# Performance work log

Measured on AMD Instinct MI355X. Metric: run time of the kernel, lower is better.

## Reference

```python
import jax, jax.numpy as jnp
import numpy as np


def setup_inputs() -> dict:
    key = jax.random.key(0)
    k1, k2, k3 = jax.random.split(key, 3)
    B, T, S, D = 8, 2048, 2048, 512
    main_input = jax.random.normal(k1, (B, T, D), dtype=jnp.float32)
    attn_input = jax.random.normal(k2, (B, S, D), dtype=jnp.float32)
    # f_input is a torch Linear(D, D): y = x @ W_f.T + b_f
    W_f = jax.random.normal(k3, (D, D), dtype=jnp.float32) * (1.0 / np.sqrt(D))
    b_f = jnp.zeros((D,), dtype=jnp.float32)
    return {"main_input": main_input, "attn_input": attn_input, "W_f": W_f, "b_f": b_f}


def reference(main_input, attn_input, W_f, b_f):
    # keys: f_input applied to each attn word  [B,S,D]
    keys = jnp.einsum("bsd,ed->bse", attn_input, W_f) + b_f
    # scores[b,t,s] = keys[b,s,:] . main_input[b,t,:]
    scores = jnp.einsum("bse,bte->bts", keys, main_input)
    attn = jax.nn.softmax(scores, axis=-1)  # softmax over attn words S
    # weighted sum of RAW attn_input (values are unprojected)
    out = jnp.einsum("bts,bsd->btd", attn, attn_input)
    return out
```

## Files before the change

### kernel.cpp

```cpp
#include <hip/hip_runtime.h>
#include <math.h>

#define B_  8
#define T_  2048
#define S_  2048
#define D_  512

typedef _Float16 half8   __attribute__((ext_vector_type(8)));
typedef _Float16 half4_t __attribute__((ext_vector_type(4)));
typedef float    floatx4 __attribute__((ext_vector_type(4)));

__device__ __forceinline__ floatx4 mfma16(half8 a, half8 b, floatx4 c) {
  return __builtin_amdgcn_mfma_f32_16x16x32_f16(a, b, c, 0, 0, 0);
}

__device__ __forceinline__ void async16(void* lds, const void* g) {
  __builtin_amdgcn_global_load_lds(
      (const __attribute__((address_space(1))) void*)g,
      (__attribute__((address_space(3))) void*)lds, 16, 0, 0);
}

__device__ __forceinline__ void bar_lds() {
  __builtin_amdgcn_sched_barrier(0);
  asm volatile("s_waitcnt lgkmcnt(0)" ::: "memory");
  __builtin_amdgcn_s_barrier();
  __builtin_amdgcn_sched_barrier(0);
}

__global__ __launch_bounds__(256) void transpose_cast_kernel(
    const float* __restrict__ attn, _Float16* __restrict__ Vt) {
  __shared__ _Float16 tile[32][33];
  const int tx = threadIdx.x, ty = threadIdx.y;
  const int b = blockIdx.z, s0 = blockIdx.y * 32, d0 = blockIdx.x * 32;
  const float* src = attn + ((size_t)b * S_ + s0) * D_ + d0;
#pragma unroll
  for (int i = 0; i < 4; ++i) {
    int s = ty + i * 8;
    tile[tx][s] = (_Float16)src[(size_t)s * D_ + tx];
  }
  __syncthreads();
  _Float16* dst = Vt + ((size_t)b * D_ + d0) * S_ + s0;
#pragma unroll
  for (int i = 0; i < 4; ++i) {
    int d = ty + i * 8;
    dst[(size_t)d * S_ + tx] = tile[d][tx];
  }
}

__global__ __launch_bounds__(512, 2) void keys_gemm_kernel(
    const float* __restrict__ X, const float* __restrict__ W,
    const float* __restrict__ bias, _Float16* __restrict__ K16) {
  __shared__ alignas(16) _Float16 Xs[128][72];
  __shared__ alignas(16) _Float16 Ws[128][72];
  const int t = threadIdx.x;
  const int wave = t >> 6, lane = t & 63, q = lane >> 4, n = lane & 15;
  const int wm = wave >> 2, wn = wave & 3;
  const int m0 = blockIdx.x * 128, n0 = blockIdx.y * 128;

  floatx4 acc[4][2];
#pragma unroll
  for (int i = 0; i < 4; ++i)
#pragma unroll
    for (int j = 0; j < 2; ++j) {
      floatx4 z = {0.f, 0.f, 0.f, 0.f};
      acc[i][j] = z;
    }

  for (int kc = 0; kc < 8; ++kc) {
    const int k0 = kc * 64;
#pragma unroll
    for (int i = 0; i < 4; ++i) {
      int seg = i * 512 + t;
      int row = seg >> 4, c4 = (seg & 15) * 4;
      floatx4 xv = *(const floatx4*)&X[(size_t)(m0 + row) * D_ + k0 + c4];
      floatx4 wv = *(const floatx4*)&W[(size_t)(n0 + row) * D_ + k0 + c4];
      half4_t xh, wh;
#pragma unroll
      for (int j = 0; j < 4; ++j) { xh[j] = (_Float16)xv[j]; wh[j] = (_Float16)wv[j]; }
      *(half4_t*)&Xs[row][c4] = xh;
      *(half4_t*)&Ws[row][c4] = wh;
    }
    __syncthreads();
#pragma unroll
    for (int kk = 0; kk < 2; ++kk) {
      half8 a[4], bb[2];
#pragma unroll
      for (int mt = 0; mt < 4; ++mt)
        a[mt] = *(const half8*)&Xs[wm * 64 + mt * 16 + n][kk * 32 + q * 8];
#pragma unroll
      for (int nt = 0; nt < 2; ++nt)
        bb[nt] = *(const half8*)&Ws[wn * 32 + nt * 16 + n][kk * 32 + q * 8];
#pragma unroll
      for (int mt = 0; mt < 4; ++mt)
#pragma unroll
        for (int nt = 0; nt < 2; ++nt)
          acc[mt][nt] = mfma16(a[mt], bb[nt], acc[mt][nt]);
    }
    __syncthreads();
  }

#pragma unroll
  for (int nt = 0; nt < 2; ++nt) {
    int col = n0 + wn * 32 + nt * 16 + n;
    float bv = bias[col];
#pragma unroll
    for (int mt = 0; mt < 4; ++mt)
#pragma unroll
      for (int r = 0; r < 4; ++r) {
        int row = m0 + wm * 64 + mt * 16 + q * 4 + r;
        K16[(size_t)row * D_ + col] = (_Float16)(acc[mt][nt][r] + bv);
      }
  }
}

__global__ __launch_bounds__(512, 2) void flash_kernel(
    const float* __restrict__ Qf, const _Float16* __restrict__ K16,
    const _Float16* __restrict__ Vt, float* __restrict__ out) {
  __shared__ alignas(16) _Float16 Klds[2][32][512];
  __shared__ alignas(16) _Float16 Vlds[2][512][32];
  __shared__ alignas(16) _Float16 Pscr[4][16][40];
  __shared__ float Mscr[4][2][16];

  const int t = threadIdx.x;
  const int w = t >> 6, lane = t & 63, qd = lane >> 4, n = lane & 15;
  const int n7 = n & 7;
  const int rg = w >> 1, h = w & 1;
  const int bid = blockIdx.x;
  const int b = bid & 7, t0 = (bid >> 3) * 64;

  const _Float16* Kb = K16 + (size_t)b * S_ * D_;
  const _Float16* Vb = Vt + (size_t)b * D_ * S_;

  const int vsw = (lane & 3) ^ ((lane >> 3) & 3);
  const int ccV = qd ^ ((n >> 1) & 3);

  half8 qreg[16];
  {
    const float* qrow = Qf + ((size_t)b * T_ + t0 + rg * 16 + n) * D_;
#pragma unroll
    for (int kk = 0; kk < 16; ++kk) {
      floatx4 v0 = *(const floatx4*)&qrow[kk * 32 + qd * 8];
      floatx4 v1 = *(const floatx4*)&qrow[kk * 32 + qd * 8 + 4];
      half8 hv;
#pragma unroll
      for (int j = 0; j < 4; ++j) { hv[j] = (_Float16)v0[j]; hv[j + 4] = (_Float16)v1[j]; }
      qreg[kk] = hv;
    }
  }

  floatx4 O[17];
#pragma unroll
  for (int ng = 0; ng < 17; ++ng) {
    floatx4 z = {0.f, 0.f, 0.f, 0.f};
    O[ng] = z;
  }
  float m_st[4];
#pragma unroll
  for (int r = 0; r < 4; ++r) m_st[r] = -1e30f;

  half8 ones8;
#pragma unroll
  for (int j = 0; j < 8; ++j) ones8[j] = (_Float16)1.0f;

#pragma unroll
  for (int i = 0; i < 4; ++i) {
    int row = w * 4 + i;
    async16(&Klds[0][row][0], Kb + (size_t)row * D_ + ((lane ^ (row & 7)) * 8));
  }
#pragma unroll
  for (int i = 0; i < 4; ++i) {
    int d0 = (w * 4 + i) * 16;
    async16(&Vlds[0][d0][0], Vb + (size_t)(d0 + (lane >> 2)) * S_ + vsw * 8);
  }
  __syncthreads();

  for (int st = 0; st < S_ / 32; ++st) {
    const int cur = st & 1, nxt = cur ^ 1;
    const int s0 = st * 32;

    if (st < S_ / 32 - 1) {
#pragma unroll
      for (int i = 0; i < 4; ++i) {
        int row = w * 4 + i;
        async16(&Klds[nxt][row][0],
                Kb + (size_t)(s0 + 32 + row) * D_ + ((lane ^ (row & 7)) * 8));
      }
#pragma unroll
      for (int i = 0; i < 4; ++i) {
        int d0 = (w * 4 + i) * 16;
        async16(&Vlds[nxt][d0][0],
                Vb + (size_t)(d0 + (lane >> 2)) * S_ + s0 + 32 + vsw * 8);
      }
    }

    floatx4 Sa = {0.f, 0.f, 0.f, 0.f}, Sb = Sa;
#pragma unroll
    for (int kk = 0; kk < 8; ++kk) {
      int slot = (kk * 4 + qd) ^ n7;
      half8 bk = *(const half8*)&Klds[cur][h * 16 + n][slot * 8];
      Sa = mfma16(qreg[kk], bk, Sa);
    }
#pragma unroll
    for (int kk = 8; kk < 16; ++kk) {
      int slot = (kk * 4 + qd) ^ n7;
      half8 bk = *(const half8*)&Klds[cur][h * 16 + n][slot * 8];
      Sb = mfma16(qreg[kk], bk, Sb);
    }
    floatx4 Sc = Sa + Sb;

#pragma unroll
    for (int r = 0; r < 4; ++r) {
      float v = Sc[r];
      v = fmaxf(v, __shfl_xor(v, 1, 16));
      v = fmaxf(v, __shfl_xor(v, 2, 16));
      v = fmaxf(v, __shfl_xor(v, 4, 16));
      v = fmaxf(v, __shfl_xor(v, 8, 16));
      if (n == qd * 4 + r) Mscr[rg][h][n] = v;
    }
    bar_lds();

    float pm[4], need = 0.f;
#pragma unroll
    for (int r = 0; r < 4; ++r) {
      int row = qd * 4 + r;
      pm[r] = fmaxf(Mscr[rg][0][row], Mscr[rg][1][row]);
      need = fmaxf(need, pm[r] - m_st[r]);
    }
    if (__any(need > 8.f)) {
#pragma unroll
      for (int r = 0; r < 4; ++r) {
        float mn = fmaxf(m_st[r], pm[r]);
        float al = __expf(m_st[r] - mn);
        m_st[r] = mn;
#pragma unroll
        for (int ng = 0; ng < 17; ++ng) O[ng][r] *= al;
      }
    }

#pragma unroll
    for (int r = 0; r < 4; ++r) {
      float p = __expf(Sc[r] - m_st[r]);
      Pscr[rg][qd * 4 + r][h * 16 + n] = (_Float16)p;
    }
    bar_lds();

    half8 av = *(const half8*)&Pscr[rg][n][qd * 8];

#pragma unroll
    for (int ng = 0; ng < 16; ++ng) {
      half8 bv = *(const half8*)&Vlds[cur][h * 256 + ng * 16 + n][ccV * 8];
      O[ng] = mfma16(av, bv, O[ng]);
    }
    O[16] = mfma16(av, ones8, O[16]);

    if (st < S_ / 32 - 1) __syncthreads();
  }

  float* ob = out + ((size_t)b * T_ + t0 + rg * 16) * D_ + h * 256;
#pragma unroll
  for (int r = 0; r < 4; ++r) {
    float inv = 1.f / O[16][r];
    const size_t rowoff = (size_t)(qd * 4 + r) * D_;
#pragma unroll
    for (int ng = 0; ng < 16; ++ng)
      ob[rowoff + ng * 16 + n] = O[ng][r] * inv;
  }
}

extern "C" void kernel_launch(void* const* d_in, const int* in_sizes, int n_in,
                              void* d_out, int out_size, void* d_ws, size_t ws_size,
                              hipStream_t stream) {
  (void)in_sizes; (void)n_in; (void)out_size; (void)ws_size;
  const float* main_in = (const float*)d_in[0];
  const float* attn_in = (const float*)d_in[1];
  const float* W_f     = (const float*)d_in[2];
  const float* b_f     = (const float*)d_in[3];
  float* out = (float*)d_out;

  _Float16* K16 = (_Float16*)d_ws;
  _Float16* Vt  = K16 + (size_t)B_ * S_ * D_;

  transpose_cast_kernel<<<dim3(D_ / 32, S_ / 32, B_), dim3(32, 8, 1), 0, stream>>>(
      attn_in, Vt);
  keys_gemm_kernel<<<dim3((B_ * S_) / 128, D_ / 128), 512, 0, stream>>>(
      attn_in, W_f, b_f, K16);
  flash_kernel<<<(B_ * T_) / 64, 512, 0, stream>>>(main_in, K16, Vt, out);
}
```

Baseline: 288.2 us.

## Compute full 32-key score tile per wave to drop cross-wave barriers

Each wave of a pair now computes both 16-key halves of the QK^T score tile instead of splitting them across two waves. The row max is then found with in-wave shuffles only, and P is staged in a per-wave LDS buffer. This removes the two block-wide LDS barriers per KV step that were used to exchange max values and P between waves. The cost is that each wave does twice the QK MFMA work and twice the K reads from LDS, and the per-wave P buffer adds a little shared memory.

```diff
diff --git a/kernel.cpp b/kernel.cpp
--- a/kernel.cpp
+++ b/kernel.cpp
@@ -18,13 +18,6 @@
   __builtin_amdgcn_global_load_lds(
       (const __attribute__((address_space(1))) void*)g,
       (__attribute__((address_space(3))) void*)lds, 16, 0, 0);
-}
-
-__device__ __forceinline__ void bar_lds() {
-  __builtin_amdgcn_sched_barrier(0);
-  asm volatile("s_waitcnt lgkmcnt(0)" ::: "memory");
-  __builtin_amdgcn_s_barrier();
-  __builtin_amdgcn_sched_barrier(0);
 }
 
 __global__ __launch_bounds__(256) void transpose_cast_kernel(
@@ -118,8 +111,7 @@
     const _Float16* __restrict__ Vt, float* __restrict__ out) {
   __shared__ alignas(16) _Float16 Klds[2][32][512];
   __shared__ alignas(16) _Float16 Vlds[2][512][32];
-  __shared__ alignas(16) _Float16 Pscr[4][16][40];
-  __shared__ float Mscr[4][2][16];
+  __shared__ alignas(16) _Float16 Pp[8][16][40];
 
   const int t = threadIdx.x;
   const int w = t >> 6, lane = t & 63, qd = lane >> 4, n = lane & 15;
@@ -133,6 +125,8 @@
 
   const int vsw = (lane & 3) ^ ((lane >> 3) & 3);
   const int ccV = qd ^ ((n >> 1) & 3);
+  const int psw = qd & 2;
+  const int prd = (qd ^ ((n & 8) >> 2)) * 8;
 
   half8 qreg[16];
   {
@@ -193,38 +187,35 @@
       }
     }
 
-    floatx4 Sa = {0.f, 0.f, 0.f, 0.f}, Sb = Sa;
+    floatx4 Sa0 = {0.f, 0.f, 0.f, 0.f}, Sa1 = Sa0, Sb0 = Sa0, Sb1 = Sa0;
 #pragma unroll
     for (int kk = 0; kk < 8; ++kk) {
       int slot = (kk * 4 + qd) ^ n7;
-      half8 bk = *(const half8*)&Klds[cur][h * 16 + n][slot * 8];
-      Sa = mfma16(qreg[kk], bk, Sa);
+      half8 b0 = *(const half8*)&Klds[cur][n][slot * 8];
+      half8 b1 = *(const half8*)&Klds[cur][16 + n][slot * 8];
+      Sa0 = mfma16(qreg[kk], b0, Sa0);
+      Sa1 = mfma16(qreg[kk], b1, Sa1);
     }
 #pragma unroll
     for (int kk = 8; kk < 16; ++kk) {
       int slot = (kk * 4 + qd) ^ n7;
-      half8 bk = *(const half8*)&Klds[cur][h * 16 + n][slot * 8];
-      Sb = mfma16(qreg[kk], bk, Sb);
-    }
-    floatx4 Sc = Sa + Sb;
-
+      half8 b0 = *(const half8*)&Klds[cur][n][slot * 8];
+      half8 b1 = *(const half8*)&Klds[cur][16 + n][slot * 8];
+      Sb0 = mfma16(qreg[kk], b0, Sb0);
+      Sb1 = mfma16(qreg[kk], b1, Sb1);
+    }
+    floatx4 Sc0 = Sa0 + Sb0, Sc1 = Sa1 + Sb1;
+
+    float pm[4], need = 0.f;
 #pragma unroll
     for (int r = 0; r < 4; ++r) {
-      float v = Sc[r];
+      float v = fmaxf(Sc0[r], Sc1[r]);
       v = fmaxf(v, __shfl_xor(v, 1, 16));
       v = fmaxf(v, __shfl_xor(v, 2, 16));
       v = fmaxf(v, __shfl_xor(v, 4, 16));
       v = fmaxf(v, __shfl_xor(v, 8, 16));
-      if (n == qd * 4 + r) Mscr[rg][h][n] = v;
-    }
-    bar_lds();
-
-    float pm[4], need = 0.f;
-#pragma unroll
-    for (int r = 0; r < 4; ++r) {
-      int row = qd * 4 + r;
-      pm[r] = fmaxf(Mscr[rg][0][row], Mscr[rg][1][row]);
-      need = fmaxf(need, pm[r] - m_st[r]);
+      pm[r] = v;
+      need = fmaxf(need, v - m_st[r]);
     }
     if (__any(need > 8.f)) {
 #pragma unroll
@@ -239,12 +230,14 @@
 
 #pragma unroll
     for (int r = 0; r < 4; ++r) {
-      float p = __expf(Sc[r] - m_st[r]);
-      Pscr[rg][qd * 4 + r][h * 16 + n] = (_Float16)p;
-    }
-    bar_lds();
-
-    half8 av = *(const half8*)&Pscr[rg][n][qd * 8];
+      float p0 = __expf(Sc0[r] - m_st[r]);
+      float p1 = __expf(Sc1[r] - m_st[r]);
+      int sc0 = (n >> 3) ^ psw;
+      int sc1 = (2 | (n >> 3)) ^ psw;
+      Pp[w][qd * 4 + r][sc0 * 8 + n7] = (_Float16)p0;
+      Pp[w][qd * 4 + r][sc1 * 8 + n7] = (_Float16)p1;
+    }
+    half8 av = *(const half8*)&Pp[w][n][prd];
 
 #pragma unroll
     for (int ng = 0; ng < 16; ++ng) {
```

New measurement: 304.6 us. 1.06x slower.
